# Performance work log

Hardware: AMD Instinct MI355X
Metric: run time of the kernel (lower is better)

## Reference

```python
import jax, jax.numpy as jnp
import numpy as np

B, S, D, H = 2, 2048, 2048, 16
HD = D // H  # head dim = 128


def setup_inputs() -> dict:
    key = jax.random.key(0)
    ks = jax.random.split(key, 9)
    sc = 1.0 / np.sqrt(D)
    return {
        "hidden_states": jax.random.normal(ks[0], (B, S, D), jnp.float32),
        "Wq": jax.random.normal(ks[1], (D, D), jnp.float32) * sc,
        "bq": jax.random.normal(ks[2], (D,), jnp.float32) * 0.02,
        "Wk": jax.random.normal(ks[3], (D, D), jnp.float32) * sc,
        "bk": jax.random.normal(ks[4], (D,), jnp.float32) * 0.02,
        "Wv": jax.random.normal(ks[5], (D, D), jnp.float32) * sc,
        "bv": jax.random.normal(ks[6], (D,), jnp.float32) * 0.02,
        "Wo": jax.random.normal(ks[7], (D, D), jnp.float32) * sc,
        "bo": jax.random.normal(ks[8], (D,), jnp.float32) * 0.02,
    }


def _rotate_half(x):
    x1, x2 = jnp.split(x, 2, axis=-1)
    return jnp.concatenate((-x2, x1), axis=-1)


def reference(hidden_states, Wq, bq, Wk, bk, Wv, bv, Wo, bo):
    b, s, d = hidden_states.shape
    # QKV projections (torch Linear: x @ W.T + b)
    def proj(W, bias):
        y = jnp.einsum('bsd,ed->bse', hidden_states, W) + bias
        return y.reshape(b, s, H, HD).transpose(0, 2, 1, 3)  # [B,H,S,HD]
    q, k, v = proj(Wq, bq), proj(Wk, bk), proj(Wv, bv)

    # Rotary embedding tables
    inv_freq = 1.0 / (10000.0 ** (jnp.arange(0, HD, 2, dtype=jnp.float32) / HD))
    t = jnp.arange(s, dtype=jnp.float32)
    freqs = jnp.einsum('i,j->ij', t, inv_freq)          # [S, HD/2]
    emb = jnp.concatenate((freqs, freqs), axis=-1)       # [S, HD]
    cos_cached, sin_cached = jnp.cos(emb), jnp.sin(emb)
    # NOTE: source unpacks `sin, cos = rotary_emb(...)` while forward returns
    # (cos, sin) -> swap is intentional to match original math.
    sin_t, cos_t = cos_cached, sin_cached
    q = q * cos_t + _rotate_half(q) * sin_t
    k = k * cos_t + _rotate_half(k) * sin_t

    scores = jnp.einsum('bhsd,bhtd->bhst', q, k) / jnp.sqrt(jnp.float32(HD))
    probs = jax.nn.softmax(scores, axis=-1)
    ctx = jnp.einsum('bhst,bhtd->bhsd', probs, v)
    ctx = ctx.transpose(0, 2, 1, 3).reshape(b, s, d)
    return jnp.einsum('bsd,ed->bse', ctx, Wo) + bo
```

## Files before the change

### kernel.cpp

```cpp
#include <hip/hip_runtime.h>

constexpr int NH = 16;
constexpr int SEQ = 2048;
constexpr int DMODEL = 2048;
constexpr int HDIM = 128;
constexpr int NB = 2;
constexpr int MTOT = NB * SEQ;
constexpr long NEL = (long)NB * SEQ * DMODEL;
constexpr long WEL = (long)DMODEL * DMODEL;
constexpr size_t FUSED_WS = 2ul * (4 * NEL + 3 * WEL + 12288);

typedef __attribute__((ext_vector_type(8))) __bf16 bf16x8;
typedef __attribute__((ext_vector_type(4))) float f32x4;

__device__ __forceinline__ float bf2f(ushort u) {
  union { uint i; float f; } v; v.i = ((uint)u) << 16; return v.f;
}
__device__ __forceinline__ ushort f2bf(float f) {
  union { float f; uint i; } v; v.f = f;
  uint r = (v.i + 0x7FFFu + ((v.i >> 16) & 1u)) >> 16;
  return (ushort)r;
}
__device__ __forceinline__ ushort f2bf_rhu(float f) {
  union { float f; uint i; } v; v.f = f;
  return (ushort)((v.i + 0x8000u) >> 16);
}
__device__ __forceinline__ float fast_exp2(float x) {
#if __has_builtin(__builtin_amdgcn_exp2f)
  return __builtin_amdgcn_exp2f(x);
#else
  float r;
  asm volatile("v_exp_f32 %0, %1\n\ts_nop 0" : "=v"(r) : "v"(x));
  return r;
#endif
}

__global__ __launch_bounds__(256) void conv_f32_bf16(
    const float* __restrict__ s, ushort* __restrict__ d, int n4) {
  const int i = blockIdx.x * 256 + threadIdx.x;
  if (i < n4) {
    const float4 v = ((const float4*)s)[i];
    ushort4 o;
    o.x = f2bf(v.x); o.y = f2bf(v.y); o.z = f2bf(v.z); o.w = f2bf(v.w);
    ((ushort4*)d)[i] = o;
  }
}

__global__ __launch_bounds__(256) void bias_cat(
    const float* __restrict__ a, const float* __restrict__ b,
    const float* __restrict__ c, float* __restrict__ o) {
  const int i = blockIdx.x * 256 + threadIdx.x;
  o[i] = (i < 2048) ? a[i] : (i < 4096) ? b[i - 2048] : c[i - 4096];
}

#define GLDS(src, dst)                                              \
  __builtin_amdgcn_global_load_lds(                                 \
      (const __attribute__((address_space(1))) void*)(src),         \
      (__attribute__((address_space(3))) void*)(dst), 16, 0, 0)

#define BARX() __builtin_amdgcn_s_barrier()
#define WAITV(n) asm volatile("s_waitcnt vmcnt(" #n ")" ::: "memory")
#define WAITL() asm volatile("s_waitcnt lgkmcnt(0)" ::: "memory")

#define G3_STG_A(d, kt) do {                                        \
    const ushort* _s = gA + (long)(kt) * 64;                        \
    ushort* _d = smem + (d) * 8192 + w * 512;                       \
    GLDS(_s, _d);                                                   \
    GLDS(_s + 64 * (long)K, _d + 4096);                             \
  } while (0)

#define G3_STG_B(d, j, kt) do {                                     \
    const ushort* _s = gB + (long)(j) * 128 * K + (long)(kt) * 64;  \
    ushort* _d = smem + 16384 + (d) * 24576 + (j) * 8192 + w * 512; \
    GLDS(_s, _d);                                                   \
    GLDS(_s + 64 * (long)K, _d + 4096);                             \
  } while (0)

#define G3_LDA(d) do {                                              \
    const ushort* _p = smem + (d) * 8192 + (wm * 64 + l16) * 64;    \
    _Pragma("unroll")                                               \
    for (int _i = 0; _i < 4; _i++) {                                \
      afr[_i][0] = *(const bf16x8*)(_p + _i * 1024 + sw0);          \
      afr[_i][1] = *(const bf16x8*)(_p + _i * 1024 + sw1);          \
    }                                                               \
  } while (0)

#define G3_LDB(d, j, s) do {                                        \
    const ushort* _p = smem + 16384 + (d) * 24576 + (j) * 8192 +    \
                       (wn * 32 + l16) * 64;                        \
    _Pragma("unroll")                                               \
    for (int _j = 0; _j < 2; _j++) {                                \
      bfr[s][_j][0] = *(const bf16x8*)(_p + _j * 1024 + sw0);       \
      bfr[s][_j][1] = *(const bf16x8*)(_p + _j * 1024 + sw1);       \
    }                                                               \
  } while (0)

#define G3_MMA(s, j) do {                                           \
    __builtin_amdgcn_s_setprio(1);                                  \
    _Pragma("unroll")                                               \
    for (int _i = 0; _i < 4; _i++)                                  \
      _Pragma("unroll")                                             \
      for (int _j = 0; _j < 2; _j++) {                              \
        acc[_i][(j) * 2 + _j] = __builtin_amdgcn_mfma_f32_16x16x32_bf16( \
            afr[_i][0], bfr[s][_j][0], acc[_i][(j) * 2 + _j], 0, 0, 0);  \
        acc[_i][(j) * 2 + _j] = __builtin_amdgcn_mfma_f32_16x16x32_bf16( \
            afr[_i][1], bfr[s][_j][1], acc[_i][(j) * 2 + _j], 0, 0, 0);  \
      }                                                             \
    __builtin_amdgcn_s_setprio(0);                                  \
  } while (0)

template <int MODE>
__global__ __launch_bounds__(512, 2) void gemm384(
    const ushort* __restrict__ A, const ushort* __restrict__ Bw,
    const float* __restrict__ bias, void* __restrict__ Cv,
    int M, int N, int K) {
  __shared__ __align__(16) ushort smem[65536];
  const int tid = threadIdx.x;
  const int w = tid >> 6, lane = tid & 63;
  const int quad = lane >> 4, l16 = lane & 15;
  const int wm = w >> 2, wn = w & 3;
  const int nbm = M >> 7, nbn = N / 384;
  const int rm = nbm >> 1, rn = nbn >> 2;
  const int xcd = blockIdx.x & 7, loc = blockIdx.x >> 3;
  const int bm = (xcd >> 2) * rm + (loc % rm);
  const int bn = (xcd & 3) * rn + (loc / rm);
  const int m0 = bm << 7, n0 = bn * 384;
  const int KT = K >> 6;

  const int srow = tid >> 3;
  const int scol = (((tid & 7) ^ ((tid >> 3) & 7)) << 3);
  const ushort* gA = A + (long)(m0 + srow) * K + scol;
  const ushort* gB = Bw + (long)(n0 + srow) * K + scol;
  const int sw0 = ((quad ^ (l16 & 7)) << 3);
  const int sw1 = (((4 + quad) ^ (l16 & 7)) << 3);

  f32x4 acc[4][6] = {};
  bf16x8 afr[4][2];
  bf16x8 bfr[2][2][2];

  G3_STG_A(0, 0);
  G3_STG_B(0, 0, 0); G3_STG_B(0, 1, 0); G3_STG_B(0, 2, 0);
  G3_STG_A(1, 1);
  G3_STG_B(1, 0, 1); G3_STG_B(1, 1, 1);
  WAITV(10);
  BARX();
  G3_LDA(0); G3_LDB(0, 0, 0);
  WAITL();
  BARX();

  for (int t = 0; t < KT; t += 2) {
    const int e2 = (t + 2 < KT) ? t + 2 : 0;
    const int e3 = (t + 3 < KT) ? t + 3 : 1;
    G3_STG_B(1, 2, t + 1);
    G3_STG_A(0, e2);
    WAITV(10); BARX(); WAITL();
    G3_MMA(0, 0);
    G3_LDB(0, 1, 1);
    BARX();
    G3_STG_B(0, 0, e2);
    BARX(); WAITL();
    G3_MMA(1, 1);
    G3_LDB(0, 2, 0);
    BARX();
    G3_STG_B(0, 1, e2);
    WAITV(10); BARX(); WAITL();
    G3_MMA(0, 2);
    G3_LDA(1);
    G3_LDB(1, 0, 1);
    BARX();
    G3_STG_B(0, 2, e2);
    G3_STG_A(1, e3);
    WAITV(10); BARX(); WAITL();
    G3_MMA(1, 0);
    G3_LDB(1, 1, 0);
    BARX();
    G3_STG_B(1, 0, e3);
    BARX(); WAITL();
    G3_MMA(0, 1);
    G3_LDB(1, 2, 1);
    BARX();
    G3_STG_B(1, 1, e3);
    WAITV(10); BARX(); WAITL();
    G3_MMA(1, 2);
    G3_LDA(0);
    G3_LDB(0, 0, 0);
    BARX();
  }

#pragma unroll
  for (int i = 0; i < 4; i++) {
    const int rbase = m0 + wm * 64 + i * 16 + quad * 4;
#pragma unroll
    for (int jt = 0; jt < 3; jt++)
#pragma unroll
      for (int j = 0; j < 2; j++) {
        const int col = n0 + jt * 128 + wn * 32 + j * 16 + l16;
        const float bv = bias[col];
#pragma unroll
        for (int r = 0; r < 4; r++) {
          const int row = rbase + r;
          const float v = acc[i][jt * 2 + j][r] + bv;
          if (MODE == 0) {
            ((float*)Cv)[(long)row * N + col] = v;
          } else {
            const int b = row >> 11, s = row & (SEQ - 1);
            const int h = (col >> 7) & 15, hd = col & (HDIM - 1);
            const long off = (long)(col >> 11) * NEL +
                ((long)(b * NH + h) * SEQ + s) * HDIM + hd;
            ((ushort*)Cv)[off] = f2bf(v);
          }
        }
      }
  }
}

#define STG_A(d, kt) do {                                           \
    const ushort* _s = gA + (long)(kt) * 64;                        \
    ushort* _d = smem + (d) * 8192 + w * 512;                       \
    GLDS(_s, _d);                                                   \
    GLDS(_s + 64 * (long)K, _d + 4096);                             \
  } while (0)

#define STG_B0(d, kt) do {                                          \
    const ushort* _s = gB + (long)(kt) * 64;                        \
    ushort* _d = smem + 16384 + (d) * 16384 + w * 512;              \
    GLDS(_s, _d);                                                   \
    GLDS(_s + 64 * (long)K, _d + 4096);                             \
  } while (0)

#define STG_B1(d, kt) do {                                          \
    const ushort* _s = gB + 128 * (long)K + (long)(kt) * 64;        \
    ushort* _d = smem + 16384 + (d) * 16384 + 8192 + w * 512;       \
    GLDS(_s, _d);                                                   \
    GLDS(_s + 64 * (long)K, _d + 4096);                             \
  } while (0)

#define LDAF(d) do {                                                \
    const ushort* _p = smem + (d) * 8192 + (wm * 64 + l16) * 64;    \
    _Pragma("unroll")                                               \
    for (int _i = 0; _i < 4; _i++) {                                \
      afr[_i][0] = *(const bf16x8*)(_p + _i * 1024 + sw0);          \
      afr[_i][1] = *(const bf16x8*)(_p + _i * 1024 + sw1);          \
    }                                                               \
  } while (0)

#define LDBF(d, nh) do {                                            \
    const ushort* _p = smem + 16384 + (d) * 16384 +                 \
                       ((nh) * 128 + wn * 32 + l16) * 64;           \
    _Pragma("unroll")                                               \
    for (int _j = 0; _j < 2; _j++) {                                \
      bfr[nh][_j][0] = *(const bf16x8*)(_p + _j * 1024 + sw0);      \
      bfr[nh][_j][1] = *(const bf16x8*)(_p + _j * 1024 + sw1);      \
    }                                                               \
  } while (0)

#define MMAP(nh) do {                                               \
    __builtin_amdgcn_s_setprio(1);                                  \
    _Pragma("unroll")                                               \
    for (int _i = 0; _i < 4; _i++)                                  \
      _Pragma("unroll")                                             \
      for (int _j = 0; _j < 2; _j++) {                              \
        acc[_i][(nh) * 2 + _j] = __builtin_amdgcn_mfma_f32_16x16x32_bf16( \
            afr[_i][0], bfr[nh][_j][0], acc[_i][(nh) * 2 + _j], 0, 0, 0); \
        acc[_i][(nh) * 2 + _j] = __builtin_amdgcn_mfma_f32_16x16x32_bf16( \
            afr[_i][1], bfr[nh][_j][1], acc[_i][(nh) * 2 + _j], 0, 0, 0); \
      }                                                             \
    __builtin_amdgcn_s_setprio(0);                                  \
  } while (0)

template <int MODE>
__global__ __launch_bounds__(512, 2) void gemm128(
    const ushort* __restrict__ A, const ushort* __restrict__ Bw,
    const float* __restrict__ bias, void* __restrict__ Cv,
    int M, int N, int K) {
  __shared__ __align__(16) ushort smem[49152];
  const int tid = threadIdx.x;
  const int w = tid >> 6, lane = tid & 63;
  const int quad = lane >> 4, l16 = lane & 15;
  const int wm = w >> 2, wn = w & 3;
  const int nbm = M >> 7, nbn = N >> 8;
  const int rm = nbm >> 1, rn = nbn >> 2;
  const int xcd = blockIdx.x & 7, loc = blockIdx.x >> 3;
  const int bm = (xcd >> 2) * rm + (loc % rm);
  const int bn = (xcd & 3) * rn + (loc / rm);
  const int m0 = bm << 7, n0 = bn << 8;
  const int KT = K >> 6;

  const int srow = tid >> 3;
  const int scol = (((tid & 7) ^ ((tid >> 3) & 7)) << 3);
  const ushort* gA = A + (long)(m0 + srow) * K + scol;
  const ushort* gB = Bw + (long)(n0 + srow) * K + scol;
  const int sw0 = ((quad ^ (l16 & 7)) << 3);
  const int sw1 = (((4 + quad) ^ (l16 & 7)) << 3);

  f32x4 acc[4][4] = {};
  bf16x8 afr[4][2];
  bf16x8 bfr[2][2][2];

  STG_B1(0, 0);
  STG_A(0, 0); STG_B0(0, 0);
  STG_A(1, 1); STG_B0(1, 1);
  WAITV(4);
  BARX();
  LDAF(0); LDBF(0, 0);
  WAITL();
  BARX();

  for (int t = 0; t < KT; t++) {
    const int d = t & 1, nd = d ^ 1;
    const int c1 = (t + 1 < KT) ? t + 1 : 0;
    const int c2 = (t + 2 < KT) ? t + 2 : (t + 2 - KT);
    STG_B1(nd, c1);
    STG_A(d, c2);
    WAITV(8);
    BARX();
    WAITL();
    MMAP(0);
    LDBF(d, 1);
    BARX();
    STG_B0(d, c2);
    WAITV(6);
    BARX();
    WAITL();
    MMAP(1);
    LDAF(nd); LDBF(nd, 0);
    BARX();
  }

#pragma unroll
  for (int i = 0; i < 4; i++) {
    const int rbase = m0 + wm * 64 + i * 16 + quad * 4;
#pragma unroll
    for (int nh = 0; nh < 2; nh++)
#pragma unroll
      for (int j = 0; j < 2; j++) {
        const int col = n0 + nh * 128 + wn * 32 + j * 16 + l16;
        const float bv = bias[col];
#pragma unroll
        for (int r = 0; r < 4; r++) {
          const int row = rbase + r;
          const float v = acc[i][nh * 2 + j][r] + bv;
          if (MODE == 0) {
            ((float*)Cv)[(long)row * N + col] = v;
          } else {
            const int b = row >> 11, s = row & (SEQ - 1);
            const int h = (col >> 7) & 15, hd = col & (HDIM - 1);
            const long off = (long)(col >> 11) * NEL +
                ((long)(b * NH + h) * SEQ + s) * HDIM + hd;
            ((ushort*)Cv)[off] = f2bf(v);
          }
        }
      }
  }
}

__global__ __launch_bounds__(256) void rope_qk(ushort* Q, ushort* Kt) {
  const int gid = blockIdx.x * 256 + threadIdx.x;
  const int n = gid & 4194303;
  const bool isK = (gid >= 4194304);
  ushort* ptr = isK ? Kt : Q;
  const float qs = isK ? 1.0f : 0.12751743f;
  const int p = n & 63;
  const int s = (n >> 6) & (SEQ - 1);
  const int bh = n >> 17;
  const long idx = (long)bh * (SEQ * HDIM) + (long)s * HDIM + p;
  const float invf_rev =
      fast_exp2(-(float)p * 0.2076205059304601f) * 0.15915494309189535f;
  float rev = (float)s * invf_rev;
  rev -= floorf(rev);
  const float sn = __builtin_amdgcn_sinf(rev);
  const float cs = __builtin_amdgcn_cosf(rev);
  const float x1 = bf2f(ptr[idx]);
  const float x2 = bf2f(ptr[idx + 64]);
  ptr[idx]      = f2bf((x1 * sn - x2 * cs) * qs);
  ptr[idx + 64] = f2bf((x2 * sn + x1 * cs) * qs);
}

__global__ __launch_bounds__(256) void transpose_v(const ushort* __restrict__ V,
                                                   ushort* __restrict__ VT) {
  __shared__ ushort lT[64 * 65];
  const int bh = blockIdx.x >> 6;
  const int rem = blockIdx.x & 63;
  const int t0 = (rem >> 1) << 6, d0 = (rem & 1) << 6;
  const ushort* vb = V + (long)bh * (SEQ * HDIM);
  ushort* ob = VT + (long)bh * (SEQ * HDIM);
  const int tid = threadIdx.x;
#pragma unroll
  for (int it = 0; it < 16; it++) {
    const int idx = it * 256 + tid;
    const int r = idx >> 6, c = idx & 63;
    lT[c * 65 + r] = vb[(long)(t0 + r) * HDIM + d0 + c];
  }
  __syncthreads();
#pragma unroll
  for (int it = 0; it < 16; it++) {
    const int idx = it * 256 + tid;
    const int r = idx >> 6, c = idx & 63;
    ob[(long)(d0 + r) * SEQ + t0 + c] = lT[r * 65 + c];
  }
}

__global__ __launch_bounds__(256, 2) void attn(const ushort* __restrict__ Q,
                                               const ushort* __restrict__ Kp,
                                               const ushort* __restrict__ VT,
                                               ushort* __restrict__ ctx) {
  __shared__ __align__(16) ushort smem[40960];
  const int tid = threadIdx.x;
  const int wave = tid >> 6, lane = tid & 63;
  const int quad = lane >> 4, l16 = lane & 15;
  const int xcd = blockIdx.x & 7, loc = blockIdx.x >> 3;
  const int bh = xcd * 4 + (loc >> 5), qt = loc & 31;
  const long hb = (long)bh * (SEQ * HDIM);
  const int b = bh >> 4, h = bh & 15;
  const int qh = wave & 1, th = wave >> 1;
  ushort* myP = smem + 35840 + wave * (32 * 40);

  bf16x8 qa[2][4];
#pragma unroll
  for (int qq = 0; qq < 2; qq++)
#pragma unroll
    for (int c = 0; c < 4; c++)
      qa[qq][c] = *(const bf16x8*)(
          Q + hb + (long)(qt * 64 + qh * 32 + qq * 16 + l16) * HDIM +
          c * 32 + (quad << 3));

  f32x4 o[2][8] = {};
  f32x4 lacc[2] = {};
  bf16x8 ones;
#pragma unroll
  for (int i = 0; i < 8; i++) ones[i] = (__bf16)1.0f;

  const ushort* kSrc = Kp + hb + (long)(tid >> 4) * HDIM + (tid & 15) * 8;
  const ushort* vSrc = VT + hb + (long)(tid >> 3) * SEQ + (tid & 7) * 8;
  const int kOff = (tid >> 4) * 136 + (tid & 15) * 8;
  const int vOff = (tid >> 3) * 72 + (tid & 7) * 8;

  {
    bf16x8 kR[4], vR[4];
#pragma unroll
    for (int it = 0; it < 4; it++) {
      kR[it] = *(const bf16x8*)(kSrc + (long)it * (16 * HDIM));
      vR[it] = *(const bf16x8*)(vSrc + (long)it * (32 * SEQ));
    }
    kSrc += 64 * HDIM; vSrc += 64;
#pragma unroll
    for (int it = 0; it < 4; it++) {
      *(bf16x8*)(smem + kOff + it * (16 * 136)) = kR[it];
      *(bf16x8*)(smem + 17408 + vOff + it * (32 * 72)) = vR[it];
    }
  }
  __syncthreads();

  for (int t0 = 0; t0 < SEQ; t0 += 64) {
    const int cur = (t0 >> 6) & 1;
    ushort* cK = cur ? smem + 8704 : smem;
    ushort* cV = cur ? smem + 26624 : smem + 17408;
    ushort* nK = cur ? smem : smem + 8704;
    ushort* nV = cur ? smem + 17408 : smem + 26624;
    const bool more = (t0 + 64 < SEQ);

    bf16x8 kR[4], vR[4];
    if (more) {
#pragma unroll
      for (int it = 0; it < 4; it++) {
        kR[it] = *(const bf16x8*)(kSrc + (long)it * (16 * HDIM));
        vR[it] = *(const bf16x8*)(vSrc + (long)it * (32 * SEQ));
      }
      kSrc += 64 * HDIM; vSrc += 64;
    }

    const ushort* kRow = cK + (th * 32 + l16) * 136 + (quad << 3);
    f32x4 st[2][2] = {};
    __builtin_amdgcn_s_setprio(1);
#pragma unroll
    for (int kc = 0; kc < 4; kc++)
#pragma unroll
      for (int tt = 0; tt < 2; tt++) {
        const bf16x8 ka = *(const bf16x8*)(kRow + tt * (16 * 136) + kc * 32);
#pragma unroll
        for (int qq = 0; qq < 2; qq++)
          st[tt][qq] = __builtin_amdgcn_mfma_f32_16x16x32_bf16(
              ka, qa[qq][kc], st[tt][qq], 0, 0, 0);
      }
    __builtin_amdgcn_s_setprio(0);

    ushort* pW = myP + l16 * 40 + (quad << 2);
#pragma unroll
    for (int qq = 0; qq < 2; qq++)
#pragma unroll
      for (int tt = 0; tt < 2; tt++) {
        ushort4 pk;
        pk.x = f2bf_rhu(fast_exp2(st[tt][qq][0]));
        pk.y = f2bf_rhu(fast_exp2(st[tt][qq][1]));
        pk.z = f2bf_rhu(fast_exp2(st[tt][qq][2]));
        pk.w = f2bf_rhu(fast_exp2(st[tt][qq][3]));
        *(ushort4*)(pW + qq * (16 * 40) + tt * 16) = pk;
      }
    WAITL();
    __builtin_amdgcn_sched_barrier(0);

    const ushort* pRow = myP + l16 * 40 + (quad << 3);
    const ushort* vRow = cV + l16 * 72 + th * 32 + (quad << 3);
    bf16x8 pa[2];
    __builtin_amdgcn_s_setprio(1);
#pragma unroll
    for (int qq = 0; qq < 2; qq++) {
      pa[qq] = *(const bf16x8*)(pRow + qq * (16 * 40));
      lacc[qq] = __builtin_amdgcn_mfma_f32_16x16x32_bf16(
          pa[qq], ones, lacc[qq], 0, 0, 0);
    }
#pragma unroll
    for (int nt = 0; nt < 8; nt++) {
      const bf16x8 vb = *(const bf16x8*)(vRow + nt * (16 * 72));
#pragma unroll
      for (int qq = 0; qq < 2; qq++)
        o[qq][nt] = __builtin_amdgcn_mfma_f32_16x16x32_bf16(
            pa[qq], vb, o[qq][nt], 0, 0, 0);
    }
    __builtin_amdgcn_s_setprio(0);

    if (more) {
#pragma unroll
      for (int it = 0; it < 4; it++) {
        *(bf16x8*)(nK + kOff + it * (16 * 136)) = kR[it];
        *(bf16x8*)(nV + vOff + it * (32 * 72)) = vR[it];
      }
    }
    __syncthreads();
  }

  float* mb = (float*)smem;
  if (wave >= 2) {
    float* p = mb + ((wave - 2) * 64 + lane) * 73;
#pragma unroll
    for (int qq = 0; qq < 2; qq++) {
#pragma unroll
      for (int nt = 0; nt < 8; nt++)
#pragma unroll
        for (int r = 0; r < 4; r++) p[qq * 32 + nt * 4 + r] = o[qq][nt][r];
#pragma unroll
      for (int r = 0; r < 4; r++) p[64 + qq * 4 + r] = lacc[qq][r];
    }
  }
  __syncthreads();
  if (wave < 2) {
    const float* p = mb + (wave * 64 + lane) * 73;
#pragma unroll
    for (int qq = 0; qq < 2; qq++) {
#pragma unroll
      for (int nt = 0; nt < 8; nt++)
#pragma unroll
        for (int r = 0; r < 4; r++) o[qq][nt][r] += p[qq * 32 + nt * 4 + r];
#pragma unroll
      for (int r = 0; r < 4; r++) lacc[qq][r] += p[64 + qq * 4 + r];
    }
#pragma unroll
    for (int qq = 0; qq < 2; qq++)
#pragma unroll
      for (int r = 0; r < 4; r++) {
        const float inv = 1.0f / lacc[qq][r];
        const int s = qt * 64 + qh * 32 + qq * 16 + quad * 4 + r;
        const long base = ((long)(b * SEQ + s)) * DMODEL + h * HDIM;
#pragma unroll
        for (int nt = 0; nt < 8; nt++)
          ctx[base + nt * 16 + l16] = f2bf(o[qq][nt][r] * inv);
      }
  }
}

extern "C" void kernel_launch(void* const* d_in, const int* in_sizes, int n_in,
                              void* d_out, int out_size, void* d_ws, size_t ws_size,
                              hipStream_t stream) {
  const float* hid = (const float*)d_in[0];
  const float* Wq = (const float*)d_in[1];
  const float* bq = (const float*)d_in[2];
  const float* Wk = (const float*)d_in[3];
  const float* bk = (const float*)d_in[4];
  const float* Wv = (const float*)d_in[5];
  const float* bv = (const float*)d_in[6];
  const float* Wo = (const float*)d_in[7];
  const float* bo = (const float*)d_in[8];
  float* out = (float*)d_out;
  ushort* ws = (ushort*)d_ws;

  ushort* qw   = ws;
  ushort* kw   = ws + NEL;
  ushort* vw   = ws + 2 * NEL;
  ushort* hidB = ws + 3 * NEL;
  ushort* wB   = ws + 4 * NEL;

  dim3 blk(256);
  dim3 blkG(512);
  conv_f32_bf16<<<(int)(NEL / 4 / 256), blk, 0, stream>>>(hid, hidB, NEL / 4);

  if (ws_size >= FUSED_WS) {
    conv_f32_bf16<<<(int)(WEL / 4 / 256), blk, 0, stream>>>(Wq, wB, WEL / 4);
    conv_f32_bf16<<<(int)(WEL / 4 / 256), blk, 0, stream>>>(Wk, wB + WEL, WEL / 4);
    conv_f32_bf16<<<(int)(WEL / 4 / 256), blk, 0, stream>>>(Wv, wB + 2 * WEL, WEL / 4);
    float* bc = (float*)(wB + 3 * WEL);
    bias_cat<<<24, blk, 0, stream>>>(bq, bk, bv, bc);
    gemm384<1><<<512, blkG, 0, stream>>>(hidB, wB, bc, qw, MTOT, 3 * DMODEL, DMODEL);
  } else {
    conv_f32_bf16<<<(int)(WEL / 4 / 256), blk, 0, stream>>>(Wq, wB, WEL / 4);
    gemm128<1><<<256, blkG, 0, stream>>>(hidB, wB, bq, qw, MTOT, DMODEL, DMODEL);
    conv_f32_bf16<<<(int)(WEL / 4 / 256), blk, 0, stream>>>(Wk, wB, WEL / 4);
    gemm128<1><<<256, blkG, 0, stream>>>(hidB, wB, bk, kw, MTOT, DMODEL, DMODEL);
    conv_f32_bf16<<<(int)(WEL / 4 / 256), blk, 0, stream>>>(Wv, wB, WEL / 4);
    gemm128<1><<<256, blkG, 0, stream>>>(hidB, wB, bv, vw, MTOT, DMODEL, DMODEL);
  }

  rope_qk<<<32768, blk, 0, stream>>>(qw, kw);

  ushort* vtw = hidB;
  transpose_v<<<2048, blk, 0, stream>>>(vw, vtw);

  ushort* cw = vw;
  attn<<<1024, blk, 0, stream>>>(qw, kw, vtw, cw);

  conv_f32_bf16<<<(int)(WEL / 4 / 256), blk, 0, stream>>>(Wo, wB, WEL / 4);
  gemm128<0><<<256, blkG, 0, stream>>>(cw, wB, bo, out, MTOT, DMODEL, DMODEL);
}
```

Baseline: 403.3 us.

## Split attention work across waves by key/head-dim slices with shared P tile

Result: slower. 452.1 us (+12.1%).

```diff
diff --git a/kernel.cpp b/kernel.cpp
--- a/kernel.cpp
+++ b/kernel.cpp
@@ -400,172 +400,99 @@
   }
 }
 
-__global__ __launch_bounds__(256, 2) void attn(const ushort* __restrict__ Q,
+__global__ __launch_bounds__(256, 3) void attn(const ushort* __restrict__ Q,
                                                const ushort* __restrict__ Kp,
                                                const ushort* __restrict__ VT,
                                                ushort* __restrict__ ctx) {
-  __shared__ __align__(16) ushort smem[40960];
+  __shared__ __align__(16) ushort lP[2][64 * 72];
   const int tid = threadIdx.x;
-  const int wave = tid >> 6, lane = tid & 63;
+  const int w = tid >> 6, lane = tid & 63;
   const int quad = lane >> 4, l16 = lane & 15;
   const int xcd = blockIdx.x & 7, loc = blockIdx.x >> 3;
   const int bh = xcd * 4 + (loc >> 5), qt = loc & 31;
   const long hb = (long)bh * (SEQ * HDIM);
   const int b = bh >> 4, h = bh & 15;
-  const int qh = wave & 1, th = wave >> 1;
-  ushort* myP = smem + 35840 + wave * (32 * 40);
-
-  bf16x8 qa[2][4];
-#pragma unroll
-  for (int qq = 0; qq < 2; qq++)
-#pragma unroll
-    for (int c = 0; c < 4; c++)
-      qa[qq][c] = *(const bf16x8*)(
-          Q + hb + (long)(qt * 64 + qh * 32 + qq * 16 + l16) * HDIM +
-          c * 32 + (quad << 3));
-
-  f32x4 o[2][8] = {};
-  f32x4 lacc[2] = {};
+
+  bf16x8 qa[4][4];
+#pragma unroll
+  for (int qq = 0; qq < 4; qq++)
+#pragma unroll
+    for (int kc = 0; kc < 4; kc++)
+      qa[qq][kc] = *(const bf16x8*)(
+          Q + hb + (long)(qt * 64 + qq * 16 + l16) * HDIM + kc * 32 +
+          (quad << 3));
+
+  f32x4 o[4][2] = {};
+  f32x4 lacc[4] = {};
   bf16x8 ones;
 #pragma unroll
   for (int i = 0; i < 8; i++) ones[i] = (__bf16)1.0f;
 
-  const ushort* kSrc = Kp + hb + (long)(tid >> 4) * HDIM + (tid & 15) * 8;
-  const ushort* vSrc = VT + hb + (long)(tid >> 3) * SEQ + (tid & 7) * 8;
-  const int kOff = (tid >> 4) * 136 + (tid & 15) * 8;
-  const int vOff = (tid >> 3) * 72 + (tid & 7) * 8;
-
-  {
-    bf16x8 kR[4], vR[4];
-#pragma unroll
-    for (int it = 0; it < 4; it++) {
-      kR[it] = *(const bf16x8*)(kSrc + (long)it * (16 * HDIM));
-      vR[it] = *(const bf16x8*)(vSrc + (long)it * (32 * SEQ));
+  const ushort* kW = Kp + hb + (long)(w * 16 + l16) * HDIM + (quad << 3);
+  const ushort* vW = VT + hb + (long)(w * 32 + l16) * SEQ + (quad << 3);
+
+  for (int t0 = 0; t0 < SEQ; t0 += 64) {
+    ushort* Pb = lP[(t0 >> 6) & 1];
+
+    bf16x8 vf[2][2];
+#pragma unroll
+    for (int nt = 0; nt < 2; nt++)
+#pragma unroll
+      for (int kc = 0; kc < 2; kc++)
+        vf[nt][kc] = *(const bf16x8*)(vW + (long)nt * (16 * SEQ) + t0 + kc * 32);
+
+    f32x4 st[4] = {};
+#pragma unroll
+    for (int kc = 0; kc < 4; kc++) {
+      const bf16x8 kf = *(const bf16x8*)(kW + (long)t0 * HDIM + kc * 32);
+#pragma unroll
+      for (int qq = 0; qq < 4; qq++)
+        st[qq] = __builtin_amdgcn_mfma_f32_16x16x32_bf16(
+            kf, qa[qq][kc], st[qq], 0, 0, 0);
     }
-    kSrc += 64 * HDIM; vSrc += 64;
-#pragma unroll
-    for (int it = 0; it < 4; it++) {
-      *(bf16x8*)(smem + kOff + it * (16 * 136)) = kR[it];
-      *(bf16x8*)(smem + 17408 + vOff + it * (32 * 72)) = vR[it];
+
+    ushort* pW = Pb + l16 * 72 + w * 16 + (quad << 2);
+#pragma unroll
+    for (int qq = 0; qq < 4; qq++) {
+      ushort4 pk;
+      pk.x = f2bf_rhu(fast_exp2(st[qq][0]));
+      pk.y = f2bf_rhu(fast_exp2(st[qq][1]));
+      pk.z = f2bf_rhu(fast_exp2(st[qq][2]));
+      pk.w = f2bf_rhu(fast_exp2(st[qq][3]));
+      *(ushort4*)(pW + qq * (16 * 72)) = pk;
     }
-  }
-  __syncthreads();
-
-  for (int t0 = 0; t0 < SEQ; t0 += 64) {
-    const int cur = (t0 >> 6) & 1;
-    ushort* cK = cur ? smem + 8704 : smem;
-    ushort* cV = cur ? smem + 26624 : smem + 17408;
-    ushort* nK = cur ? smem : smem + 8704;
-    ushort* nV = cur ? smem + 17408 : smem + 26624;
-    const bool more = (t0 + 64 < SEQ);
-
-    bf16x8 kR[4], vR[4];
-    if (more) {
-#pragma unroll
-      for (int it = 0; it < 4; it++) {
-        kR[it] = *(const bf16x8*)(kSrc + (long)it * (16 * HDIM));
-        vR[it] = *(const bf16x8*)(vSrc + (long)it * (32 * SEQ));
-      }
-      kSrc += 64 * HDIM; vSrc += 64;
-    }
-
-    const ushort* kRow = cK + (th * 32 + l16) * 136 + (quad << 3);
-    f32x4 st[2][2] = {};
-    __builtin_amdgcn_s_setprio(1);
-#pragma unroll
-    for (int kc = 0; kc < 4; kc++)
-#pragma unroll
-      for (int tt = 0; tt < 2; tt++) {
-        const bf16x8 ka = *(const bf16x8*)(kRow + tt * (16 * 136) + kc * 32);
-#pragma unroll
-        for (int qq = 0; qq < 2; qq++)
-          st[tt][qq] = __builtin_amdgcn_mfma_f32_16x16x32_bf16(
-              ka, qa[qq][kc], st[tt][qq], 0, 0, 0);
-      }
-    __builtin_amdgcn_s_setprio(0);
-
-    ushort* pW = myP + l16 * 40 + (quad << 2);
-#pragma unroll
-    for (int qq = 0; qq < 2; qq++)
-#pragma unroll
-      for (int tt = 0; tt < 2; tt++) {
-        ushort4 pk;
-        pk.x = f2bf_rhu(fast_exp2(st[tt][qq][0]));
-        pk.y = f2bf_rhu(fast_exp2(st[tt][qq][1]));
-        pk.z = f2bf_rhu(fast_exp2(st[tt][qq][2]));
-        pk.w = f2bf_rhu(fast_exp2(st[tt][qq][3]));
-        *(ushort4*)(pW + qq * (16 * 40) + tt * 16) = pk;
-      }
-    WAITL();
-    __builtin_amdgcn_sched_barrier(0);
-
-    const ushort* pRow = myP + l16 * 40 + (quad << 3);
-    const ushort* vRow = cV + l16 * 72 + th * 32 + (quad << 3);
-    bf16x8 pa[2];
-    __builtin_amdgcn_s_setprio(1);
-#pragma unroll
-    for (int qq = 0; qq < 2; qq++) {
-      pa[qq] = *(const bf16x8*)(pRow + qq * (16 * 40));
+    __syncthreads();
+
+#pragma unroll
+    for (int qq = 0; qq < 4; qq++) {
+      const ushort* pR = Pb + (qq * 16 + l16) * 72 + (quad << 3);
+      const bf16x8 pa0 = *(const bf16x8*)(pR);
+      const bf16x8 pa1 = *(const bf16x8*)(pR + 32);
       lacc[qq] = __builtin_amdgcn_mfma_f32_16x16x32_bf16(
-          pa[qq], ones, lacc[qq], 0, 0, 0);
-    }
-#pragma unroll
-    for (int nt = 0; nt < 8; nt++) {
-      const bf16x8 vb = *(const bf16x8*)(vRow + nt * (16 * 72));
-#pragma unroll
-      for (int qq = 0; qq < 2; qq++)
+          pa0, ones, lacc[qq], 0, 0, 0);
+      lacc[qq] = __builtin_amdgcn_mfma_f32_16x16x32_bf16(
+          pa1, ones, lacc[qq], 0, 0, 0);
+#pragma unroll
+      for (int nt = 0; nt < 2; nt++) {
         o[qq][nt] = __builtin_amdgcn_mfma_f32_16x16x32_bf16(
-            pa[qq], vb, o[qq][nt], 0, 0, 0);
-    }
-    __builtin_amdgcn_s_setprio(0);
-
-    if (more) {
-#pragma unroll
-      for (int it = 0; it < 4; it++) {
-        *(bf16x8*)(nK + kOff + it * (16 * 136)) = kR[it];
-        *(bf16x8*)(nV + vOff + it * (32 * 72)) = vR[it];
+            pa0, vf[nt][0], o[qq][nt], 0, 0, 0);
+        o[qq][nt] = __builtin_amdgcn_mfma_f32_16x16x32_bf16(
+            pa1, vf[nt][1], o[qq][nt], 0, 0, 0);
       }
     }
-    __syncthreads();
-  }
-
-  float* mb = (float*)smem;
-  if (wave >= 2) {
-    float* p = mb + ((wave - 2) * 64 + lane) * 73;
-#pragma unroll
-    for (int qq = 0; qq < 2; qq++) {
-#pragma unroll
-      for (int nt = 0; nt < 8; nt++)
-#pragma unroll
-        for (int r = 0; r < 4; r++) p[qq * 32 + nt * 4 + r] = o[qq][nt][r];
-#pragma unroll
-      for (int r = 0; r < 4; r++) p[64 + qq * 4 + r] = lacc[qq][r];
+  }
+
+#pragma unroll
+  for (int qq = 0; qq < 4; qq++)
+#pragma unroll
+    for (int r = 0; r < 4; r++) {
+      const float inv = 1.0f / lacc[qq][r];
+      const int s = qt * 64 + qq * 16 + quad * 4 + r;
+      const long base = ((long)(b * SEQ + s)) * DMODEL + h * HDIM + w * 32;
+#pragma unroll
+      for (int nt = 0; nt < 2; nt++)
+        ctx[base + nt * 16 + l16] = f2bf(o[qq][nt][r] * inv);
     }
-  }
-  __syncthreads();
-  if (wave < 2) {
-    const float* p = mb + (wave * 64 + lane) * 73;
-#pragma unroll
-    for (int qq = 0; qq < 2; qq++) {
-#pragma unroll
-      for (int nt = 0; nt < 8; nt++)
-#pragma unroll
-        for (int r = 0; r < 4; r++) o[qq][nt][r] += p[qq * 32 + nt * 4 + r];
-#pragma unroll
-      for (int r = 0; r < 4; r++) lacc[qq][r] += p[64 + qq * 4 + r];
-    }
-#pragma unroll
-    for (int qq = 0; qq < 2; qq++)
-#pragma unroll
-      for (int r = 0; r < 4; r++) {
-        const float inv = 1.0f / lacc[qq][r];
-        const int s = qt * 64 + qh * 32 + qq * 16 + quad * 4 + r;
-        const long base = ((long)(b * SEQ + s)) * DMODEL + h * HDIM;
-#pragma unroll
-        for (int nt = 0; nt < 8; nt++)
-          ctx[base + nt * 16 + l16] = f2bf(o[qq][nt][r] * inv);
-      }
-  }
 }
 
 extern "C" void kernel_launch(void* const* d_in, const int* in_sizes, int n_in,
```
